# Performance work log

Hardware: AMD Instinct MI355X
Metric: run time of the kernel (lower is better)

Reference implementation:

```python
import jax, jax.numpy as jnp
import numpy as np

B, C, H, W = 2, 128, 96, 96
HEADS, DHEAD, WIN = 4, 32, 5
INNER = HEADS * DHEAD
PAD = WIN // 2


def setup_inputs() -> dict:
    key = jax.random.key(0)
    k1, k2, k3, k4, k5 = jax.random.split(key, 5)
    s = 1.0 / np.sqrt(C)
    return {
        "x": jax.random.normal(k1, (B, C, H, W), dtype=jnp.float32),
        "wq": jax.random.normal(k2, (INNER, C), dtype=jnp.float32) * s,
        "wk": jax.random.normal(k3, (INNER, C), dtype=jnp.float32) * s,
        "wv": jax.random.normal(k4, (INNER, C), dtype=jnp.float32) * s,
        "wproj": jax.random.normal(k5, (C, INNER), dtype=jnp.float32) * s,
    }


def _windows(t):
    # same neighborhood ordering as F.unfold (row-major over kernel offsets).
    tp = jnp.pad(t, ((0, 0), (0, 0), (0, 0), (PAD, PAD), (PAD, PAD)))
    wins = [tp[:, :, :, di:di + H, dj:dj + W]
            for di in range(WIN) for dj in range(WIN)]
    return jnp.stack(wins, axis=3)


def reference(x, wq, wk, wv, wproj):
    # 1x1 convs == per-pixel linear maps
    q = jnp.einsum('oc,bcxy->boxy', wq, x).reshape(B, HEADS, DHEAD, H, W)
    k = jnp.einsum('oc,bcxy->boxy', wk, x).reshape(B, HEADS, DHEAD, H, W)
    v = jnp.einsum('oc,bcxy->boxy', wv, x).reshape(B, HEADS, DHEAD, H, W)

    k_win = _windows(k)  # (B,h,d,25,H,W)
    v_win = _windows(v)

    scale = 1.0 / np.sqrt(DHEAD)
    attn = jnp.einsum('bhdxy,bhdkxy->bhkxy', q, k_win) * scale
    attn = jax.nn.softmax(attn, axis=2)  # softmax over the 25 window positions
    out = jnp.einsum('bhkxy,bhdkxy->bhdxy', attn, v_win)

    out = out.reshape(B, INNER, H, W)
    return jnp.einsum('co,boxy->bcxy', wproj, out)
```

## Files before the change

kernel.cpp:

```cpp
#include <hip/hip_runtime.h>
#include <hip/hip_fp16.h>

#define PP 9216

typedef _Float16 f16x8 __attribute__((ext_vector_type(8)));
typedef _Float16 f16x4 __attribute__((ext_vector_type(4)));
typedef float    f32x4 __attribute__((ext_vector_type(4)));

__device__ __forceinline__ int swz128(int row, int hc) {
    return row * 128 + (((hc >> 3) ^ (row & 15)) << 3) + (hc & 7);
}
__device__ __forceinline__ int swz64(int row, int hc) {
    return row * 64 + (((hc >> 3) ^ (row & 7)) << 3) + (hc & 7);
}

__device__ __forceinline__ f16x8 zero8() {
    f16x8 z;
    #pragma unroll
    for (int e = 0; e < 8; e++) z[e] = (_Float16)0;
    return z;
}

__global__ __launch_bounds__(256) void prep_w(
    const float* __restrict__ wq, const float* __restrict__ wk,
    const float* __restrict__ wv, const float* __restrict__ wp,
    _Float16* __restrict__ wqkv16, _Float16* __restrict__ wp16)
{
    int e = (blockIdx.x * 256 + threadIdx.x) * 4;
    const float* src;
    _Float16* dst;
    if (e < 49152) {
        int o = e >> 7;
        src = (o < 128) ? (wq + (size_t)o * 128)
            : (o < 256) ? (wk + (size_t)(o - 128) * 128)
                        : (wv + (size_t)(o - 256) * 128);
        src += (e & 127);
        dst = wqkv16 + e;
    } else {
        int j = e - 49152;
        src = wp + j;
        dst = wp16 + j;
    }
    float4 v = *(const float4*)src;
    f16x4 h;
    h[0] = (_Float16)v.x; h[1] = (_Float16)v.y;
    h[2] = (_Float16)v.z; h[3] = (_Float16)v.w;
    *(f16x4*)dst = h;
}

__global__ __launch_bounds__(256) void qkv_gemm(
    const float* __restrict__ x, const _Float16* __restrict__ wqkv,
    _Float16* __restrict__ qkvout)
{
    __shared__ __align__(16) char smem[43008];
    _Float16* sX   = (_Float16*)smem;
    _Float16* sEpi = (_Float16*)(smem + 16384);

    const int t = threadIdx.x;
    const int w = t >> 6, lane = t & 63, lm = lane & 15, quad = lane >> 4;
    const int b = blockIdx.z;
    const int p0 = blockIdx.x * 64;
    const int nbase = blockIdx.y * 192;

    const float* xb = x + (size_t)b * 128 * PP;
    _Float16* qout = qkvout + (size_t)b * PP * 384;

    {
        const int px = t & 63;
        const int c0 = (t >> 6) * 32;
        #pragma unroll
        for (int i = 0; i < 32; i++) {
            float v = xb[(size_t)(c0 + i) * PP + p0 + px];
            sX[swz128(px, c0 + i)] = (_Float16)v;
        }
    }
    __syncthreads();

    const int ms0 = (w & 1) * 32;
    const int nw = (w >> 1) * 96;

    f16x8 A[2][4];
    #pragma unroll
    for (int ms = 0; ms < 2; ms++)
        #pragma unroll
        for (int kc = 0; kc < 4; kc++)
            A[ms][kc] = *(const f16x8*)(sX + swz128(ms0 + ms * 16 + lm, kc * 32 + quad * 8));

    _Float16* strip = sEpi + w * 3328;
    #pragma unroll
    for (int nt = 0; nt < 6; nt++) {
        const int o = nbase + nw + nt * 16 + lm;
        const _Float16* wr = wqkv + (size_t)o * 128;
        f16x8 Bf[4];
        #pragma unroll
        for (int kc = 0; kc < 4; kc++)
            Bf[kc] = *(const f16x8*)(wr + kc * 32 + quad * 8);
        #pragma unroll
        for (int ms = 0; ms < 2; ms++) {
            f32x4 acc = {0.f, 0.f, 0.f, 0.f};
            #pragma unroll
            for (int kc = 0; kc < 4; kc++)
                acc = __builtin_amdgcn_mfma_f32_16x16x32_f16(A[ms][kc], Bf[kc], acc, 0, 0, 0);
            #pragma unroll
            for (int r = 0; r < 4; r++)
                strip[(ms * 16 + quad * 4 + r) * 104 + nt * 16 + lm] = (_Float16)acc[r];
        }
    }

    #pragma unroll
    for (int it = 0; it < 6; it++) {
        int idx = it * 64 + lane;
        int row = idx / 12;
        int ch  = idx % 12;
        uint4 v = *(const uint4*)&strip[row * 104 + ch * 8];
        *(uint4*)(qout + (size_t)(p0 + ms0 + row) * 384 + nbase + nw + ch * 8) = v;
    }
}

__global__ __launch_bounds__(256, 4) void attn_fused(
    const _Float16* __restrict__ qkv, const _Float16* __restrict__ wp16,
    float* __restrict__ out)
{
    __shared__ __align__(16) char smem[28672];
    const int t = threadIdx.x;
    const int w = t >> 6, lane = t & 63, lm = lane & 15, quad = lane >> 4;

    const int wgid = (blockIdx.x & 7) * 144 + (blockIdx.x >> 3);
    const int b = wgid / 576;
    const int rem = wgid - b * 576;
    const int x0 = (rem % 24) * 4, y0 = (rem / 24) * 4;

    const _Float16* qb = qkv + (size_t)b * PP * 384;
    float* ob = out + (size_t)b * 128 * PP;

    _Float16* sVT = (_Float16*)(smem + w * 6144);
    _Float16* sPh = (_Float16*)(smem + w * 6144 + 4096);
    _Float16* sAo = (_Float16*)(smem + 24576);

    {
        const int pos = lane;
        const int gy = y0 - 2 + (pos >> 3), gx = x0 - 2 + (pos & 7);
        const bool valid = ((unsigned)gy < 96u) && ((unsigned)gx < 96u);
        const int gp = valid ? (gy * 96 + gx) : 0;
        const _Float16* vsrc = qb + (size_t)gp * 384 + 256 + w * 32;
        f16x8 vv[4];
        #pragma unroll
        for (int j = 0; j < 4; j++) {
            f16x8 ld = *(const f16x8*)(vsrc + j * 8);
            vv[j] = valid ? ld : zero8();
        }
        #pragma unroll
        for (int j = 0; j < 4; j++)
            #pragma unroll
            for (int e = 0; e < 8; e++) {
                int d = j * 8 + e;
                sVT[d * 64 + ((((pos >> 3)) ^ (d & 7)) << 3) + (pos & 7)] = vv[j][e];
            }
    }

    const int gpq = (y0 + (lm >> 2)) * 96 + x0 + (lm & 3);
    f16x8 Aq = *(const f16x8*)(qb + (size_t)gpq * 384 + w * 32 + quad * 8);

    f32x4 S[4];
    #pragma unroll
    for (int n = 0; n < 4; n++) {
        int pos = n * 16 + lm;
        int gy = y0 - 2 + (pos >> 3), gx = x0 - 2 + (pos & 7);
        bool valid = ((unsigned)gy < 96u) && ((unsigned)gx < 96u);
        int gp = valid ? (gy * 96 + gx) : 0;
        f16x8 ld = *(const f16x8*)(qb + (size_t)gp * 384 + 128 + w * 32 + quad * 8);
        f16x8 Bk = valid ? ld : zero8();
        f32x4 z = {0.f, 0.f, 0.f, 0.f};
        S[n] = __builtin_amdgcn_mfma_f32_16x16x32_f16(Aq, Bk, z, 0, 0, 0);
    }

    float inv4[4];
    {
        const float scale = 0.17677669529663689f;
        #pragma unroll
        for (int r = 0; r < 4; r++) {
            float e[4];
            float mx = -1e30f;
            #pragma unroll
            for (int n = 0; n < 4; n++) {
                int hy = n * 2 + (lm >> 3), hx = lm & 7;
                bool memb = (hy >= quad) && (hy < quad + 5) && (hx >= r) && (hx < r + 5);
                e[n] = memb ? S[n][r] * scale : -1e30f;
                mx = fmaxf(mx, e[n]);
            }
            mx = fmaxf(mx, __shfl_xor(mx, 1));
            mx = fmaxf(mx, __shfl_xor(mx, 2));
            mx = fmaxf(mx, __shfl_xor(mx, 4));
            mx = fmaxf(mx, __shfl_xor(mx, 8));
            float sum = 0.f;
            #pragma unroll
            for (int n = 0; n < 4; n++) {
                float ev = __expf(e[n] - mx);
                e[n] = ev;
                sum += ev;
            }
            sum += __shfl_xor(sum, 1);
            sum += __shfl_xor(sum, 2);
            sum += __shfl_xor(sum, 4);
            sum += __shfl_xor(sum, 8);
            inv4[r] = 1.f / sum;
            #pragma unroll
            for (int n = 0; n < 4; n++)
                sPh[swz64(quad * 4 + r, n * 16 + lm)] = (_Float16)e[n];
        }
    }

    {
        f32x4 acc2[2] = {{0.f, 0.f, 0.f, 0.f}, {0.f, 0.f, 0.f, 0.f}};
        #pragma unroll
        for (int kc = 0; kc < 2; kc++) {
            f16x8 Ap = *(const f16x8*)(sPh + swz64(lm, kc * 32 + quad * 8));
            #pragma unroll
            for (int nd = 0; nd < 2; nd++) {
                int row = nd * 16 + lm;
                int hc = kc * 32 + quad * 8;
                f16x8 Bv = *(const f16x8*)(sVT + row * 64
                               + (((hc >> 3) ^ (row & 7)) << 3) + (hc & 7));
                acc2[nd] = __builtin_amdgcn_mfma_f32_16x16x32_f16(Ap, Bv, acc2[nd], 0, 0, 0);
            }
        }
        #pragma unroll
        for (int nd = 0; nd < 2; nd++)
            #pragma unroll
            for (int r = 0; r < 4; r++)
                sAo[swz128(quad * 4 + r, w * 32 + nd * 16 + lm)] =
                    (_Float16)(acc2[nd][r] * inv4[r]);
    }
    __syncthreads();

    {
        f16x8 Bf[4];
        #pragma unroll
        for (int kc = 0; kc < 4; kc++)
            Bf[kc] = *(const f16x8*)(sAo + swz128(lm, kc * 32 + quad * 8));
        int gp = (y0 + (lm >> 2)) * 96 + x0 + (lm & 3);
        #pragma unroll
        for (int mi = 0; mi < 2; mi++) {
            const _Float16* wr = wp16 + (size_t)((w * 2 + mi) * 16 + lm) * 128;
            f32x4 acc = {0.f, 0.f, 0.f, 0.f};
            #pragma unroll
            for (int kc = 0; kc < 4; kc++)
                acc = __builtin_amdgcn_mfma_f32_16x16x32_f16(
                    *(const f16x8*)(wr + kc * 32 + quad * 8), Bf[kc], acc, 0, 0, 0);
            int c0 = (w * 2 + mi) * 16 + quad * 4;
            #pragma unroll
            for (int r = 0; r < 4; r++)
                ob[(size_t)(c0 + r) * PP + gp] = acc[r];
        }
    }
}

extern "C" void kernel_launch(void* const* d_in, const int* in_sizes, int n_in,
                              void* d_out, int out_size, void* d_ws, size_t ws_size,
                              hipStream_t stream)
{
    const float* x  = (const float*)d_in[0];
    const float* wq = (const float*)d_in[1];
    const float* wk = (const float*)d_in[2];
    const float* wv = (const float*)d_in[3];
    const float* wp = (const float*)d_in[4];
    float* out = (float*)d_out;

    _Float16* wqkv16 = (_Float16*)d_ws;
    _Float16* wp16   = wqkv16 + 49152;
    _Float16* qkvh   = wp16 + 16384;

    prep_w<<<dim3(64), 256, 0, stream>>>(wq, wk, wv, wp, wqkv16, wp16);
    qkv_gemm<<<dim3(144, 2, 2), 256, 0, stream>>>(x, wqkv16, qkvh);
    attn_fused<<<dim3(1152), 256, 0, stream>>>(qkvh, wp16, out);
}
```

Baseline: 103.4 us.

## Pack two attention tiles per 512-thread block and reuse P slab for output staging

```diff
diff --git a/kernel.cpp b/kernel.cpp
--- a/kernel.cpp
+++ b/kernel.cpp
@@ -12,6 +12,9 @@
 }
 __device__ __forceinline__ int swz64(int row, int hc) {
     return row * 64 + (((hc >> 3) ^ (row & 7)) << 3) + (hc & 7);
+}
+__device__ __forceinline__ int swz32(int row, int hc) {
+    return row * 32 + ((((hc >> 3) ^ (row & 3)) & 3) << 3) + (hc & 7);
 }
 
 __device__ __forceinline__ f16x8 zero8() {
@@ -66,12 +69,14 @@
     _Float16* qout = qkvout + (size_t)b * PP * 384;
 
     {
-        const int px = t & 63;
-        const int c0 = (t >> 6) * 32;
-        #pragma unroll
-        for (int i = 0; i < 32; i++) {
-            float v = xb[(size_t)(c0 + i) * PP + p0 + px];
-            sX[swz128(px, c0 + i)] = (_Float16)v;
+        const int px2 = (t & 31) * 2;
+        const int cb = t >> 5;
+        #pragma unroll
+        for (int i = 0; i < 16; i++) {
+            int c = cb + i * 8;
+            float2 v = *(const float2*)(xb + (size_t)c * PP + p0 + px2);
+            sX[swz128(px2,     c)] = (_Float16)v.x;
+            sX[swz128(px2 + 1, c)] = (_Float16)v.y;
         }
     }
     __syncthreads();
@@ -117,25 +122,29 @@
     }
 }
 
-__global__ __launch_bounds__(256, 4) void attn_fused(
+__global__ __launch_bounds__(512, 2) void attn_fused(
     const _Float16* __restrict__ qkv, const _Float16* __restrict__ wp16,
     float* __restrict__ out)
 {
-    __shared__ __align__(16) char smem[28672];
+    __shared__ __align__(16) char smem[49152];
     const int t = threadIdx.x;
-    const int w = t >> 6, lane = t & 63, lm = lane & 15, quad = lane >> 4;
-
-    const int wgid = (blockIdx.x & 7) * 144 + (blockIdx.x >> 3);
-    const int b = wgid / 576;
-    const int rem = wgid - b * 576;
+    const int sub = t >> 8;
+    const int tl = t & 255;
+    const int w = tl >> 6, lane = tl & 63, lm = lane & 15, quad = lane >> 4;
+
+    const int wg = (blockIdx.x & 7) * 72 + (blockIdx.x >> 3);
+    const int j = wg * 2 + sub;
+    const int b = j / 576;
+    const int rem = j - b * 576;
     const int x0 = (rem % 24) * 4, y0 = (rem / 24) * 4;
 
     const _Float16* qb = qkv + (size_t)b * PP * 384;
     float* ob = out + (size_t)b * 128 * PP;
 
-    _Float16* sVT = (_Float16*)(smem + w * 6144);
-    _Float16* sPh = (_Float16*)(smem + w * 6144 + 4096);
-    _Float16* sAo = (_Float16*)(smem + 24576);
+    char* base = smem + sub * 24576;
+    _Float16* sVT = (_Float16*)(base + w * 6144);
+    _Float16* sPh = (_Float16*)(base + w * 6144 + 4096);
+    _Float16* sAoW= (_Float16*)(base + w * 6144 + 4096);
 
     {
         const int pos = lane;
@@ -145,16 +154,16 @@
         const _Float16* vsrc = qb + (size_t)gp * 384 + 256 + w * 32;
         f16x8 vv[4];
         #pragma unroll
-        for (int j = 0; j < 4; j++) {
-            f16x8 ld = *(const f16x8*)(vsrc + j * 8);
-            vv[j] = valid ? ld : zero8();
-        }
-        #pragma unroll
-        for (int j = 0; j < 4; j++)
+        for (int jj = 0; jj < 4; jj++) {
+            f16x8 ld = *(const f16x8*)(vsrc + jj * 8);
+            vv[jj] = valid ? ld : zero8();
+        }
+        #pragma unroll
+        for (int jj = 0; jj < 4; jj++)
             #pragma unroll
             for (int e = 0; e < 8; e++) {
-                int d = j * 8 + e;
-                sVT[d * 64 + ((((pos >> 3)) ^ (d & 7)) << 3) + (pos & 7)] = vv[j][e];
+                int d = jj * 8 + e;
+                sVT[d * 64 + ((((pos >> 3)) ^ (d & 7)) << 3) + (pos & 7)] = vv[jj][e];
             }
     }
 
@@ -228,7 +237,7 @@
         for (int nd = 0; nd < 2; nd++)
             #pragma unroll
             for (int r = 0; r < 4; r++)
-                sAo[swz128(quad * 4 + r, w * 32 + nd * 16 + lm)] =
+                sAoW[swz32(quad * 4 + r, nd * 16 + lm)] =
                     (_Float16)(acc2[nd][r] * inv4[r]);
     }
     __syncthreads();
@@ -236,8 +245,10 @@
     {
         f16x8 Bf[4];
         #pragma unroll
-        for (int kc = 0; kc < 4; kc++)
-            Bf[kc] = *(const f16x8*)(sAo + swz128(lm, kc * 32 + quad * 8));
+        for (int kc = 0; kc < 4; kc++) {
+            const _Float16* slab = (const _Float16*)(base + kc * 6144 + 4096);
+            Bf[kc] = *(const f16x8*)(slab + swz32(lm, quad * 8));
+        }
         int gp = (y0 + (lm >> 2)) * 96 + x0 + (lm & 3);
         #pragma unroll
         for (int mi = 0; mi < 2; mi++) {
@@ -272,5 +283,5 @@
 
     prep_w<<<dim3(64), 256, 0, stream>>>(wq, wk, wv, wp, wqkv16, wp16);
     qkv_gemm<<<dim3(144, 2, 2), 256, 0, stream>>>(x, wqkv16, qkvh);
-    attn_fused<<<dim3(1152), 256, 0, stream>>>(qkvh, wp16, out);
-}
+    attn_fused<<<dim3(576), 512, 0, stream>>>(qkvh, wp16, out);
+}
```

Result: no change. 104.6 us (+1.1%).

## Transpose attention MFMAs so V loads go to registers directly, drop V smem

Applied to the files above, without the earlier changes.

```diff
diff --git a/kernel.cpp b/kernel.cpp
--- a/kernel.cpp
+++ b/kernel.cpp
@@ -66,12 +66,14 @@
     _Float16* qout = qkvout + (size_t)b * PP * 384;
 
     {
-        const int px = t & 63;
-        const int c0 = (t >> 6) * 32;
-        #pragma unroll
-        for (int i = 0; i < 32; i++) {
-            float v = xb[(size_t)(c0 + i) * PP + p0 + px];
-            sX[swz128(px, c0 + i)] = (_Float16)v;
+        const int px2 = (t & 31) * 2;
+        const int cb = t >> 5;
+        #pragma unroll
+        for (int i = 0; i < 16; i++) {
+            int c = cb + i * 8;
+            float2 v = *(const float2*)(xb + (size_t)c * PP + p0 + px2);
+            sX[swz128(px2,     c)] = (_Float16)v.x;
+            sX[swz128(px2 + 1, c)] = (_Float16)v.y;
         }
     }
     __syncthreads();
@@ -121,7 +123,7 @@
     const _Float16* __restrict__ qkv, const _Float16* __restrict__ wp16,
     float* __restrict__ out)
 {
-    __shared__ __align__(16) char smem[28672];
+    __shared__ __align__(16) char smem[12288];
     const int t = threadIdx.x;
     const int w = t >> 6, lane = t & 63, lm = lane & 15, quad = lane >> 4;
 
@@ -133,33 +135,11 @@
     const _Float16* qb = qkv + (size_t)b * PP * 384;
     float* ob = out + (size_t)b * 128 * PP;
 
-    _Float16* sVT = (_Float16*)(smem + w * 6144);
-    _Float16* sPh = (_Float16*)(smem + w * 6144 + 4096);
-    _Float16* sAo = (_Float16*)(smem + 24576);
-
-    {
-        const int pos = lane;
-        const int gy = y0 - 2 + (pos >> 3), gx = x0 - 2 + (pos & 7);
-        const bool valid = ((unsigned)gy < 96u) && ((unsigned)gx < 96u);
-        const int gp = valid ? (gy * 96 + gx) : 0;
-        const _Float16* vsrc = qb + (size_t)gp * 384 + 256 + w * 32;
-        f16x8 vv[4];
-        #pragma unroll
-        for (int j = 0; j < 4; j++) {
-            f16x8 ld = *(const f16x8*)(vsrc + j * 8);
-            vv[j] = valid ? ld : zero8();
-        }
-        #pragma unroll
-        for (int j = 0; j < 4; j++)
-            #pragma unroll
-            for (int e = 0; e < 8; e++) {
-                int d = j * 8 + e;
-                sVT[d * 64 + ((((pos >> 3)) ^ (d & 7)) << 3) + (pos & 7)] = vv[j][e];
-            }
-    }
+    _Float16* sPh = (_Float16*)(smem + w * 2048);
+    _Float16* sAo = (_Float16*)(smem + 8192);
 
     const int gpq = (y0 + (lm >> 2)) * 96 + x0 + (lm & 3);
-    f16x8 Aq = *(const f16x8*)(qb + (size_t)gpq * 384 + w * 32 + quad * 8);
+    f16x8 Bq = *(const f16x8*)(qb + (size_t)gpq * 384 + w * 32 + quad * 8);
 
     f32x4 S[4];
     #pragma unroll
@@ -169,67 +149,85 @@
         bool valid = ((unsigned)gy < 96u) && ((unsigned)gx < 96u);
         int gp = valid ? (gy * 96 + gx) : 0;
         f16x8 ld = *(const f16x8*)(qb + (size_t)gp * 384 + 128 + w * 32 + quad * 8);
-        f16x8 Bk = valid ? ld : zero8();
+        f16x8 Ak = valid ? ld : zero8();
         f32x4 z = {0.f, 0.f, 0.f, 0.f};
-        S[n] = __builtin_amdgcn_mfma_f32_16x16x32_f16(Aq, Bk, z, 0, 0, 0);
-    }
-
-    float inv4[4];
+        S[n] = __builtin_amdgcn_mfma_f32_16x16x32_f16(Ak, Bq, z, 0, 0, 0);
+    }
+
+    float ev[4][4];
+    float inv;
     {
         const float scale = 0.17677669529663689f;
-        #pragma unroll
-        for (int r = 0; r < 4; r++) {
-            float e[4];
-            float mx = -1e30f;
-            #pragma unroll
-            for (int n = 0; n < 4; n++) {
-                int hy = n * 2 + (lm >> 3), hx = lm & 7;
-                bool memb = (hy >= quad) && (hy < quad + 5) && (hx >= r) && (hx < r + 5);
-                e[n] = memb ? S[n][r] * scale : -1e30f;
-                mx = fmaxf(mx, e[n]);
+        const int py = lm >> 2, pxx = lm & 3;
+        float mx = -1e30f;
+        #pragma unroll
+        for (int n = 0; n < 4; n++)
+            #pragma unroll
+            for (int r = 0; r < 4; r++) {
+                int pos = n * 16 + quad * 4 + r;
+                int hy = pos >> 3, hx = pos & 7;
+                bool memb = (hy >= py) && (hy < py + 5) && (hx >= pxx) && (hx < pxx + 5);
+                float sj = memb ? S[n][r] * scale : -1e30f;
+                ev[n][r] = sj;
+                mx = fmaxf(mx, sj);
             }
-            mx = fmaxf(mx, __shfl_xor(mx, 1));
-            mx = fmaxf(mx, __shfl_xor(mx, 2));
-            mx = fmaxf(mx, __shfl_xor(mx, 4));
-            mx = fmaxf(mx, __shfl_xor(mx, 8));
-            float sum = 0.f;
-            #pragma unroll
-            for (int n = 0; n < 4; n++) {
-                float ev = __expf(e[n] - mx);
-                e[n] = ev;
-                sum += ev;
+        mx = fmaxf(mx, __shfl_xor(mx, 16));
+        mx = fmaxf(mx, __shfl_xor(mx, 32));
+        float sum = 0.f;
+        #pragma unroll
+        for (int n = 0; n < 4; n++)
+            #pragma unroll
+            for (int r = 0; r < 4; r++) {
+                float e = __expf(ev[n][r] - mx);
+                ev[n][r] = e;
+                sum += e;
             }
-            sum += __shfl_xor(sum, 1);
-            sum += __shfl_xor(sum, 2);
-            sum += __shfl_xor(sum, 4);
-            sum += __shfl_xor(sum, 8);
-            inv4[r] = 1.f / sum;
-            #pragma unroll
-            for (int n = 0; n < 4; n++)
-                sPh[swz64(quad * 4 + r, n * 16 + lm)] = (_Float16)e[n];
-        }
-    }
-
-    {
-        f32x4 acc2[2] = {{0.f, 0.f, 0.f, 0.f}, {0.f, 0.f, 0.f, 0.f}};
+        sum += __shfl_xor(sum, 16);
+        sum += __shfl_xor(sum, 32);
+        inv = 1.f / sum;
+    }
+
+    #pragma unroll
+    for (int n = 0; n < 4; n++)
+        #pragma unroll
+        for (int r = 0; r < 4; r++)
+            sPh[swz64(lm, n * 16 + quad * 4 + r)] = (_Float16)ev[n][r];
+
+    f16x8 Av[2][2];
+    #pragma unroll
+    for (int kc = 0; kc < 2; kc++) {
+        const int gy = y0 - 2 + kc * 4 + quad;
+        const bool vy = (unsigned)gy < 96u;
+        #pragma unroll
+        for (int nd = 0; nd < 2; nd++) {
+            const int ch = 256 + w * 32 + nd * 16 + lm;
+            #pragma unroll
+            for (int j = 0; j < 8; j++) {
+                int gx = x0 - 2 + j;
+                bool valid = vy && ((unsigned)gx < 96u);
+                _Float16 v = (_Float16)0;
+                if (valid) v = qb[(size_t)(gy * 96 + gx) * 384 + ch];
+                Av[nd][kc][j] = v;
+            }
+        }
+    }
+
+    {
+        f32x4 acc[2] = {{0.f, 0.f, 0.f, 0.f}, {0.f, 0.f, 0.f, 0.f}};
         #pragma unroll
         for (int kc = 0; kc < 2; kc++) {
-            f16x8 Ap = *(const f16x8*)(sPh + swz64(lm, kc * 32 + quad * 8));
-            #pragma unroll
-            for (int nd = 0; nd < 2; nd++) {
-                int row = nd * 16 + lm;
-                int hc = kc * 32 + quad * 8;
-                f16x8 Bv = *(const f16x8*)(sVT + row * 64
-                               + (((hc >> 3) ^ (row & 7)) << 3) + (hc & 7));
-                acc2[nd] = __builtin_amdgcn_mfma_f32_16x16x32_f16(Ap, Bv, acc2[nd], 0, 0, 0);
-            }
+            f16x8 Bp = *(const f16x8*)(sPh + swz64(lm, kc * 32 + quad * 8));
+            #pragma unroll
+            for (int nd = 0; nd < 2; nd++)
+                acc[nd] = __builtin_amdgcn_mfma_f32_16x16x32_f16(
+                    Av[nd][kc], Bp, acc[nd], 0, 0, 0);
         }
         #pragma unroll
         for (int nd = 0; nd < 2; nd++)
             #pragma unroll
             for (int r = 0; r < 4; r++)
-                sAo[swz128(quad * 4 + r, w * 32 + nd * 16 + lm)] =
-                    (_Float16)(acc2[nd][r] * inv4[r]);
+                sAo[swz128(lm, w * 32 + nd * 16 + quad * 4 + r)] =
+                    (_Float16)(acc[nd][r] * inv);
     }
     __syncthreads();
 
```

Result: no change. 102.3 us (-1.1%).
